# Kernel tuning notes

Measured on AMD Instinct MI355X. Metric: run time of the kernel, lower is better.

Reference implementation:

```python
import jax, jax.numpy as jnp
import numpy as np

B, S, D = 4, 1024, 768
V, L, K = 50265, 256, 4
COMMIT = 0.25
PERP_W = 0.1


def _l2n(a):
    return a * jax.lax.rsqrt(jnp.sum(a * a, axis=-1, keepdims=True) + 1e-12)


def setup_inputs() -> dict:
    key = jax.random.key(0)
    ks = jax.random.split(key, 4)
    return {
        'x': jax.random.normal(ks[0], (B, S, D), dtype=jnp.float32),
        'codebook': jax.random.normal(ks[1], (V, D), dtype=jnp.float32) * 0.02,
        'W_in': jax.random.normal(ks[2], (D, L), dtype=jnp.float32) / np.sqrt(D),
        'b_in': jnp.zeros((L,), dtype=jnp.float32),
        'W_code': jax.random.normal(ks[3], (D, L), dtype=jnp.float32) / np.sqrt(D),
        'b_code': jnp.zeros((L,), dtype=jnp.float32),
    }


def reference(x, codebook, W_in, b_in, W_code, b_code):
    # project inputs and codebook to latent space, L2-normalize
    zi = _l2n(x.reshape(-1, D) @ W_in + b_in)                 # [N, L]
    # original normalizes latent codebook twice (idempotent) then stop-grads
    zc = jax.lax.stop_gradient(_l2n(codebook @ W_code + b_code))  # [V, L]
    # squared euclidean distance: |a|^2 + |b|^2 - 2 a.b
    d = (jnp.sum(zi * zi, -1, keepdims=True)
         + jnp.sum(zc * zc, -1)[None, :]
         - 2.0 * (zi @ zc.T)).reshape(B, S, V)                # [B, S, V]
    # top-k nearest codes (exact top_k as reference for approx_min_k)
    idx = jax.lax.top_k(-d, K)[1]                             # [B, S, K] int32
    # quantize: gather codes and average over k (top_k_avg path)
    quantized = jnp.take(codebook, idx, axis=0).mean(axis=-2) # [B, S, D]
    # codebook stats without materializing [B,S,K,V] one-hot
    counts = jnp.zeros((V,), x.dtype).at[idx.reshape(-1)].add(1.0)
    codebook_usage = jnp.sum(counts > 0).astype(x.dtype) / V / K
    avg_probs = counts / (B * S * K)
    log_perp = -jnp.sum(avg_probs * jnp.log(avg_probs + 1e-10))
    perplexity = jnp.exp(log_perp)
    # train losses (quantized is stop-gradient'd before loss in original)
    q_sg = jax.lax.stop_gradient(quantized)

    def train_loss(q, t):
        e = jnp.mean((jax.lax.stop_gradient(q) - t) ** 2) * COMMIT
        ql = jnp.mean((q - jax.lax.stop_gradient(t)) ** 2)
        return e + ql

    loss = train_loss(q_sg, x)
    loss = loss + train_loss(q_sg @ W_code + b_code, x @ W_in + b_in)
    loss = loss + PERP_W * log_perp
    # straight-through estimator
    out = x + jax.lax.stop_gradient(q_sg - x)
    return out, loss, perplexity, codebook_usage
```

## Files before the change

kernel.cpp:

```cpp
#include <hip/hip_runtime.h>
#include <math.h>

#define N_TOK 4096
#define DDIM  768
#define LDIM  256
#define VNUM  50265
#define VPAD  50304
#define NT64  786
#define NGRP  16
#define QBLK  256
#define KSEL  4
#define M3    3145728

#define WS_ZI_PRE 0
#define WS_ZI     (WS_ZI_PRE + N_TOK*LDIM)
#define WS_ZC     (WS_ZI + N_TOK*LDIM)
#define WS_ZCB    (WS_ZC + VPAD*LDIM)
#define WS_QUANT  WS_ZCB
#define WS_CAND   (WS_ZCB + VPAD*LDIM/2)
#define WS_IDX    (WS_CAND + N_TOK*64)
#define WS_COUNTS (WS_IDX + N_TOK*4)
#define WS_ACCUM  (WS_COUNTS + VPAD)

typedef __attribute__((ext_vector_type(8))) short short8;
typedef __attribute__((ext_vector_type(4))) float f32x4;

__device__ __forceinline__ unsigned short f2bf(float f) {
    unsigned u = __float_as_uint(f);
    u += 0x7fffu + ((u >> 16) & 1u);
    return (unsigned short)(u >> 16);
}

__device__ __forceinline__ bool better(float v1, int i1, float v2, int i2) {
    return (v1 > v2) || (v1 == v2 && i1 < i2);
}

template<int K>
__device__ __forceinline__ void insertK(float (&v)[K], int (&ix)[K], float nv, int ni) {
    if (!better(nv, ni, v[K-1], ix[K-1])) return;
    v[K-1] = nv; ix[K-1] = ni;
    #pragma unroll
    for (int j = K-1; j > 0; j--) {
        if (better(v[j], ix[j], v[j-1], ix[j-1])) {
            float tv = v[j]; v[j] = v[j-1]; v[j-1] = tv;
            int ti = ix[j]; ix[j] = ix[j-1]; ix[j-1] = ti;
        } else break;
    }
}

__global__ __launch_bounds__(256) void gemm_k(
    const float* __restrict__ A, const float* __restrict__ W,
    const float* __restrict__ bias, float* __restrict__ out_pre,
    float* __restrict__ out_norm, unsigned short* __restrict__ out_bf,
    const float* __restrict__ target, float* __restrict__ accum_slot,
    int M, int mode)
{
    __shared__ float a_s[32*64];
    __shared__ float w_s[32*256];
    const int tid = threadIdx.x;
    const int tx = tid & 31, ty = tid >> 5;
    const int mbase = blockIdx.x * 64;

    float acc[8][8];
    #pragma unroll
    for (int i = 0; i < 8; i++)
        #pragma unroll
        for (int j = 0; j < 8; j++) acc[i][j] = 0.f;

    for (int kk = 0; kk < DDIM; kk += 32) {
        __syncthreads();
        #pragma unroll
        for (int s = 0; s < 2; s++) {
            int slot = tid + s*256;
            int row = slot >> 3, kc = (slot & 7) << 2;
            int gr = mbase + row; if (gr >= M) gr = M - 1;
            float4 v = *(const float4*)&A[(size_t)gr*DDIM + kk + kc];
            a_s[(kc+0)*64 + row] = v.x;
            a_s[(kc+1)*64 + row] = v.y;
            a_s[(kc+2)*64 + row] = v.z;
            a_s[(kc+3)*64 + row] = v.w;
        }
        #pragma unroll
        for (int s = 0; s < 8; s++) {
            int slot = tid + s*256;
            int r = slot >> 6, c = (slot & 63) << 2;
            *(float4*)&w_s[r*256 + c] = *(const float4*)&W[(size_t)(kk + r)*LDIM + c];
        }
        __syncthreads();
        #pragma unroll
        for (int k = 0; k < 32; k++) {
            float4 a0 = *(float4*)&a_s[k*64 + ty*8];
            float4 a1 = *(float4*)&a_s[k*64 + ty*8 + 4];
            float4 w0 = *(float4*)&w_s[k*256 + tx*4];
            float4 w1 = *(float4*)&w_s[k*256 + 128 + tx*4];
            float am[8] = {a0.x,a0.y,a0.z,a0.w,a1.x,a1.y,a1.z,a1.w};
            float wn[8] = {w0.x,w0.y,w0.z,w0.w,w1.x,w1.y,w1.z,w1.w};
            #pragma unroll
            for (int i = 0; i < 8; i++)
                #pragma unroll
                for (int j = 0; j < 8; j++)
                    acc[i][j] = fmaf(am[i], wn[j], acc[i][j]);
        }
    }

    float bn[8];
    #pragma unroll
    for (int j = 0; j < 8; j++) {
        int col = (j < 4) ? (tx*4 + j) : (128 + tx*4 + (j-4));
        bn[j] = bias[col];
    }
    #pragma unroll
    for (int i = 0; i < 8; i++)
        #pragma unroll
        for (int j = 0; j < 8; j++) acc[i][j] += bn[j];

    if (mode == 1) {
        #pragma unroll
        for (int i = 0; i < 8; i++) {
            int gr = mbase + ty*8 + i;
            if (gr < M) {
                *(float4*)&out_pre[(size_t)gr*LDIM + tx*4] =
                    make_float4(acc[i][0], acc[i][1], acc[i][2], acc[i][3]);
                *(float4*)&out_pre[(size_t)gr*LDIM + 128 + tx*4] =
                    make_float4(acc[i][4], acc[i][5], acc[i][6], acc[i][7]);
            }
        }
    }
    if (mode == 1 || mode == 2) {
        #pragma unroll
        for (int i = 0; i < 8; i++) {
            float s = 0.f;
            #pragma unroll
            for (int j = 0; j < 8; j++) s += acc[i][j]*acc[i][j];
            #pragma unroll
            for (int m = 16; m >= 1; m >>= 1) s += __shfl_xor(s, m, 64);
            float sc = 1.0f / sqrtf(s + 1e-12f);
            int gr = mbase + ty*8 + i;
            bool wr = (mode == 2) || (gr < M);
            if (wr) {
                float p[8];
                #pragma unroll
                for (int j = 0; j < 8; j++) p[j] = acc[i][j]*sc;
                *(float4*)&out_norm[(size_t)gr*LDIM + tx*4] = make_float4(p[0],p[1],p[2],p[3]);
                *(float4*)&out_norm[(size_t)gr*LDIM + 128 + tx*4] = make_float4(p[4],p[5],p[6],p[7]);
                if (out_bf) {
                    ushort4 b0, b1;
                    b0.x = f2bf(p[0]); b0.y = f2bf(p[1]); b0.z = f2bf(p[2]); b0.w = f2bf(p[3]);
                    b1.x = f2bf(p[4]); b1.y = f2bf(p[5]); b1.z = f2bf(p[6]); b1.w = f2bf(p[7]);
                    *(ushort4*)&out_bf[(size_t)gr*LDIM + tx*4] = b0;
                    *(ushort4*)&out_bf[(size_t)gr*LDIM + 128 + tx*4] = b1;
                }
            }
        }
    }
    if (mode == 3) {
        float ls = 0.f;
        #pragma unroll
        for (int i = 0; i < 8; i++) {
            int gr = mbase + ty*8 + i;
            if (gr < M) {
                #pragma unroll
                for (int j = 0; j < 8; j++) {
                    int col = (j < 4) ? (tx*4 + j) : (128 + tx*4 + (j-4));
                    float dd = acc[i][j] - target[(size_t)gr*LDIM + col];
                    ls = fmaf(dd, dd, ls);
                }
            }
        }
        #pragma unroll
        for (int off = 32; off >= 1; off >>= 1) ls += __shfl_down(ls, off, 64);
        __syncthreads();
        if ((tid & 63) == 0) a_s[tid >> 6] = ls;
        __syncthreads();
        if (tid == 0) atomicAdd(accum_slot, a_s[0]+a_s[1]+a_s[2]+a_s[3]);
    }
}


__device__ __forceinline__ void stage_chunk(
    const unsigned short* __restrict__ zcb, unsigned char* smem,
    int ci, int wave, int lane, int g)
{
    const int T  = g + (ci >> 2) * NGRP;
    const int kc = ci & 3;
    const int r_local = wave*8 + (lane >> 3);
    const int sg = (lane & 7) ^ (lane >> 3);
    const unsigned short* gp = zcb + (size_t)(T*64 + r_local)*LDIM + kc*64 + sg*8;
    unsigned char* lp = smem + (ci & 3)*8192 + wave*1024 + lane*16;
    __builtin_amdgcn_global_load_lds(
        (const __attribute__((address_space(1))) void*)gp,
        (__attribute__((address_space(3))) void*)lp, 16, 0, 0);
}

__global__ __launch_bounds__(512, 2) void filter_kernel(
    const float* __restrict__ zi, const unsigned short* __restrict__ zcb,
    int* __restrict__ cand)
{
    __shared__ unsigned char smem[32768];
    const int tid = threadIdx.x;
    const int wave = tid >> 6, lane = tid & 63;
    const int l15 = lane & 15, l4 = lane >> 4;
    const int qbase = blockIdx.x * QBLK + wave * 32;
    const int g = blockIdx.y;

    short8 afrag[2][8];
    #pragma unroll
    for (int qt = 0; qt < 2; qt++)
        #pragma unroll
        for (int ks = 0; ks < 8; ks++) {
            const float* src = zi + (size_t)(qbase + qt*16 + l15)*LDIM + ks*32 + l4*8;
            float4 v0 = *(const float4*)src;
            float4 v1 = *(const float4*)(src + 4);
            short8 a;
            a[0] = (short)f2bf(v0.x); a[1] = (short)f2bf(v0.y);
            a[2] = (short)f2bf(v0.z); a[3] = (short)f2bf(v0.w);
            a[4] = (short)f2bf(v1.x); a[5] = (short)f2bf(v1.y);
            a[6] = (short)f2bf(v1.z); a[7] = (short)f2bf(v1.w);
            afrag[qt][ks] = a;
        }

    float tv[2][4][3]; int tix[2][4][3];
    #pragma unroll
    for (int qt = 0; qt < 2; qt++)
        #pragma unroll
        for (int rr = 0; rr < 4; rr++)
            #pragma unroll
            for (int j = 0; j < 3; j++) { tv[qt][rr][j] = -1e30f; tix[qt][rr][j] = 0x7fffffff; }

    f32x4 acc[2][4];
    #pragma unroll
    for (int qt = 0; qt < 2; qt++)
        #pragma unroll
        for (int tc = 0; tc < 4; tc++) acc[qt][tc] = (f32x4)(0.f);

    const int nct = (g < 2) ? 50 : 49;
    const int NCk = nct * 4;

    stage_chunk(zcb, smem, 0, wave, lane, g);
    stage_chunk(zcb, smem, 1, wave, lane, g);
    stage_chunk(zcb, smem, 2, wave, lane, g);

    for (int ci = 0; ci < NCk; ci++) {
        __builtin_amdgcn_s_waitcnt(0x0F72);
        __builtin_amdgcn_s_barrier();
        asm volatile("" ::: "memory");
        int nx = ci + 3; if (nx >= NCk) nx -= NCk;
        stage_chunk(zcb, smem, nx, wave, lane, g);

        const unsigned short* lb = (const unsigned short*)(smem + (ci & 3)*8192);
        const int kc = ci & 3;
        #pragma unroll
        for (int ks2 = 0; ks2 < 2; ks2++) {
            const int kf = kc*2 + ks2;
            #pragma unroll
            for (int tc = 0; tc < 4; tc++) {
                const int c = tc*16 + l15;
                const int slot = (ks2*4 + l4) ^ (c & 7);
                const short8 b = *(const short8*)&lb[c*64 + slot*8];
                acc[0][tc] = __builtin_amdgcn_mfma_f32_16x16x32_bf16(afrag[0][kf], b, acc[0][tc], 0, 0, 0);
                acc[1][tc] = __builtin_amdgcn_mfma_f32_16x16x32_bf16(afrag[1][kf], b, acc[1][tc], 0, 0, 0);
            }
        }

        if ((ci & 3) == 3) {
            const int T = g + (ci >> 2)*NGRP;
            #pragma unroll
            for (int tc = 0; tc < 4; tc++) {
                const int col = T*64 + tc*16 + l15;
                const bool ok = col < VNUM;
                #pragma unroll
                for (int qt = 0; qt < 2; qt++) {
                    #pragma unroll
                    for (int rr = 0; rr < 4; rr++) {
                        float v = acc[qt][tc][rr];
                        if (ok) insertK<3>(tv[qt][rr], tix[qt][rr], v, col);
                    }
                    acc[qt][tc] = (f32x4)(0.f);
                }
            }
        }
    }

    #pragma unroll
    for (int qt = 0; qt < 2; qt++)
        #pragma unroll
        for (int rr = 0; rr < 4; rr++) {
            float mv[4] = { tv[qt][rr][0], tv[qt][rr][1], tv[qt][rr][2], -1e30f };
            int   mi[4] = { tix[qt][rr][0], tix[qt][rr][1], tix[qt][rr][2], 0x7fffffff };
            #pragma unroll
            for (int m = 1; m < 16; m <<= 1) {
                float ov[4]; int oi[4];
                #pragma unroll
                for (int s = 0; s < 4; s++) {
                    ov[s] = __shfl_xor(mv[s], m, 64);
                    oi[s] = __shfl_xor(mi[s], m, 64);
                }
                #pragma unroll
                for (int s = 0; s < 4; s++) insertK<4>(mv, mi, ov[s], oi[s]);
            }
            if (l15 == 0) {
                const int q = qbase + qt*16 + l4*4 + rr;
                #pragma unroll
                for (int j = 0; j < 4; j++) cand[(size_t)q*64 + g*4 + j] = mi[j];
            }
        }
}

__global__ __launch_bounds__(256) void rescore_kernel(
    const float* __restrict__ zi, const float* __restrict__ zc,
    const int* __restrict__ cand, int* __restrict__ idx4)
{
    __shared__ float zi_s[256];
    __shared__ float sval[64];
    __shared__ int   sidx[64];
    const int q = blockIdx.x;
    const int t = threadIdx.x;
    if (t < 64) *(float4*)&zi_s[t*4] = *(const float4*)&zi[(size_t)q*LDIM + t*4];
    __syncthreads();

    const int j = t >> 2, l4 = t & 3;
    int idx = cand[(size_t)q*64 + j];
    const bool valid = (unsigned)idx < (unsigned)VNUM;
    const float* r = zc + (size_t)(valid ? idx : 0)*LDIM;
    float dot = 0.f, nsq = 0.f;
    #pragma unroll
    for (int i = 0; i < 16; i++) {
        float4 v = *(const float4*)&r[i*16 + l4*4];
        float4 z = *(const float4*)&zi_s[i*16 + l4*4];
        dot = fmaf(v.x, z.x, fmaf(v.y, z.y, fmaf(v.z, z.z, fmaf(v.w, z.w, dot))));
        nsq = fmaf(v.x, v.x, fmaf(v.y, v.y, fmaf(v.z, v.z, fmaf(v.w, v.w, nsq))));
    }
    dot += __shfl_xor(dot, 1, 64); dot += __shfl_xor(dot, 2, 64);
    nsq += __shfl_xor(nsq, 1, 64); nsq += __shfl_xor(nsq, 2, 64);
    const float sc = valid ? (dot - 0.5f*nsq) : -1e30f;
    if (l4 == 0) { sval[j] = sc; sidx[j] = valid ? idx : 0x7fffffff; }
    __syncthreads();

    if (t < 64) {
        float v[4] = {-1e30f, -1e30f, -1e30f, -1e30f};
        int ix[4] = {0x7fffffff, 0x7fffffff, 0x7fffffff, 0x7fffffff};
        insertK<4>(v, ix, sval[t], sidx[t]);
        #pragma unroll
        for (int m = 1; m < 64; m <<= 1) {
            float ov[4]; int oi[4];
            #pragma unroll
            for (int s = 0; s < 4; s++) {
                ov[s] = __shfl_xor(v[s], m, 64);
                oi[s] = __shfl_xor(ix[s], m, 64);
            }
            #pragma unroll
            for (int s = 0; s < 4; s++) insertK<4>(v, ix, ov[s], oi[s]);
        }
        if (t == 0) {
            #pragma unroll
            for (int s = 0; s < 4; s++) idx4[q*4 + s] = ix[s];
        }
    }
}

__global__ __launch_bounds__(192) void gather_kernel(
    const float* __restrict__ x, const float* __restrict__ cb,
    const int* __restrict__ idx4, float* __restrict__ quant,
    float* __restrict__ out, float* __restrict__ counts,
    float* __restrict__ accum)
{
    __shared__ float red[3];
    const int n = blockIdx.x;
    const int t = threadIdx.x;
    const int i0 = idx4[n*4+0], i1 = idx4[n*4+1], i2 = idx4[n*4+2], i3 = idx4[n*4+3];
    if (t < 4) atomicAdd(&counts[idx4[n*4+t]], 1.0f);
    const int d = t*4;
    float4 c0 = *(const float4*)&cb[(size_t)i0*DDIM + d];
    float4 c1 = *(const float4*)&cb[(size_t)i1*DDIM + d];
    float4 c2 = *(const float4*)&cb[(size_t)i2*DDIM + d];
    float4 c3 = *(const float4*)&cb[(size_t)i3*DDIM + d];
    float4 xv = *(const float4*)&x[(size_t)n*DDIM + d];
    float4 qv;
    qv.x = (((c0.x + c1.x) + c2.x) + c3.x) * 0.25f;
    qv.y = (((c0.y + c1.y) + c2.y) + c3.y) * 0.25f;
    qv.z = (((c0.z + c1.z) + c2.z) + c3.z) * 0.25f;
    qv.w = (((c0.w + c1.w) + c2.w) + c3.w) * 0.25f;
    float4 o;
    o.x = xv.x + (qv.x - xv.x);
    o.y = xv.y + (qv.y - xv.y);
    o.z = xv.z + (qv.z - xv.z);
    o.w = xv.w + (qv.w - xv.w);
    *(float4*)&quant[(size_t)n*DDIM + d] = qv;
    *(float4*)&out[(size_t)n*DDIM + d] = o;
    float d0 = qv.x - xv.x, d1 = qv.y - xv.y, d2 = qv.z - xv.z, d3 = qv.w - xv.w;
    float ls = d0*d0 + d1*d1 + d2*d2 + d3*d3;
    #pragma unroll
    for (int off = 32; off >= 1; off >>= 1) ls += __shfl_down(ls, off, 64);
    if ((t & 63) == 0) red[t >> 6] = ls;
    __syncthreads();
    if (t == 0) atomicAdd(accum, red[0] + red[1] + red[2]);
}

__global__ __launch_bounds__(256) void stats_kernel(
    const float* __restrict__ counts, float* __restrict__ accum)
{
    __shared__ float redE[4], redN[4];
    int v = blockIdx.x*256 + threadIdx.x;
    float ent = 0.f, nnz = 0.f;
    if (v < VNUM) {
        float c = counts[v];
        if (c > 0.f) {
            float p = c * (1.0f/16384.0f);
            ent = p * logf(p + 1e-10f);
            nnz = 1.f;
        }
    }
    #pragma unroll
    for (int off = 32; off >= 1; off >>= 1) {
        ent += __shfl_down(ent, off, 64);
        nnz += __shfl_down(nnz, off, 64);
    }
    int t = threadIdx.x;
    if ((t & 63) == 0) { redE[t>>6] = ent; redN[t>>6] = nnz; }
    __syncthreads();
    if (t == 0) {
        atomicAdd(accum+2, redE[0]+redE[1]+redE[2]+redE[3]);
        atomicAdd(accum+3, redN[0]+redN[1]+redN[2]+redN[3]);
    }
}

__global__ void final_kernel(const float* __restrict__ accum, float* __restrict__ out)
{
    float logp = -accum[2];
    float m1 = accum[0] * (1.0f / (float)M3);
    float m2 = accum[1] * (1.0f / (float)(N_TOK*LDIM));
    float loss = (m1*0.25f + m1) + (m2*0.25f + m2) + 0.1f*logp;
    out[M3+0] = loss;
    out[M3+1] = expf(logp);
    out[M3+2] = (accum[3] / (float)VNUM) / (float)KSEL;
}

extern "C" void kernel_launch(void* const* d_in, const int* in_sizes, int n_in,
                              void* d_out, int out_size, void* d_ws, size_t ws_size,
                              hipStream_t stream)
{
    const float* x      = (const float*)d_in[0];
    const float* cb     = (const float*)d_in[1];
    const float* W_in   = (const float*)d_in[2];
    const float* b_in   = (const float*)d_in[3];
    const float* W_code = (const float*)d_in[4];
    const float* b_code = (const float*)d_in[5];
    float* out = (float*)d_out;
    float* w   = (float*)d_ws;

    float* zi_pre = w + WS_ZI_PRE;
    float* zi     = w + WS_ZI;
    float* zc     = w + WS_ZC;
    unsigned short* zcb = (unsigned short*)(w + WS_ZCB);
    float* quant  = w + WS_QUANT;
    int*   cand   = (int*)(w + WS_CAND);
    int*   idx4   = (int*)(w + WS_IDX);
    float* counts = w + WS_COUNTS;
    float* accum  = w + WS_ACCUM;

    hipMemsetAsync(counts, 0, (VPAD + 8)*sizeof(float), stream);

    gemm_k<<<N_TOK/64, 256, 0, stream>>>(x, W_in, b_in, zi_pre, zi, nullptr,
                                         nullptr, nullptr, N_TOK, 1);
    gemm_k<<<VPAD/64, 256, 0, stream>>>(cb, W_code, b_code, nullptr, zc, zcb,
                                        nullptr, nullptr, VNUM, 2);
    filter_kernel<<<dim3(N_TOK/QBLK, NGRP), 512, 0, stream>>>(zi, zcb, cand);
    rescore_kernel<<<N_TOK, 256, 0, stream>>>(zi, zc, cand, idx4);
    gather_kernel<<<N_TOK, 192, 0, stream>>>(x, cb, idx4, quant, out, counts, accum);
    stats_kernel<<<(VNUM + 255)/256, 256, 0, stream>>>(counts, accum);
    gemm_k<<<N_TOK/64, 256, 0, stream>>>(quant, W_code, b_code, nullptr, nullptr, nullptr,
                                         zi_pre, accum+1, N_TOK, 3);
    final_kernel<<<1, 1, 0, stream>>>(accum, out);
}
```

Measured before the change: 1.269 ms.

## Pre-swizzle codebook bf16 tiles and use register-staged double-buffered LDS in filter

The codebook projection GEMM now writes bf16 latents already in the per-chunk swizzled 64x64 tile layout, so each filter chunk becomes one contiguous 8KB block. The filter kernel drops the 4-deep async global_load_lds pipeline in favour of a 2-buffer LDS ring fed through registers, with two barriers per chunk. The input projection also emits a bf16 copy of the normalized latents, so the filter loads A fragments directly instead of converting from fp32. This trades the async direct-to-LDS path for simpler, fully coalesced loads, at the cost of more barriers and a shallower prefetch.

Result: faster. 1.240 ms (-2.2%).

```diff
diff --git a/kernel.cpp b/kernel.cpp
--- a/kernel.cpp
+++ b/kernel.cpp
@@ -14,7 +14,8 @@
 
 #define WS_ZI_PRE 0
 #define WS_ZI     (WS_ZI_PRE + N_TOK*LDIM)
-#define WS_ZC     (WS_ZI + N_TOK*LDIM)
+#define WS_ZIB    (WS_ZI + N_TOK*LDIM)
+#define WS_ZC     (WS_ZIB + N_TOK*LDIM/2)
 #define WS_ZCB    (WS_ZC + VPAD*LDIM)
 #define WS_QUANT  WS_ZCB
 #define WS_CAND   (WS_ZCB + VPAD*LDIM/2)
@@ -147,8 +148,20 @@
                     ushort4 b0, b1;
                     b0.x = f2bf(p[0]); b0.y = f2bf(p[1]); b0.z = f2bf(p[2]); b0.w = f2bf(p[3]);
                     b1.x = f2bf(p[4]); b1.y = f2bf(p[5]); b1.z = f2bf(p[6]); b1.w = f2bf(p[7]);
-                    *(ushort4*)&out_bf[(size_t)gr*LDIM + tx*4] = b0;
-                    *(ushort4*)&out_bf[(size_t)gr*LDIM + 128 + tx*4] = b1;
+                    if (mode == 1) {
+                        *(ushort4*)&out_bf[(size_t)gr*LDIM + tx*4] = b0;
+                        *(ushort4*)&out_bf[(size_t)gr*LDIM + 128 + tx*4] = b1;
+                    } else {
+                        const int T = gr >> 6, c = gr & 63;
+                        #pragma unroll
+                        for (int h = 0; h < 2; h++) {
+                            const int k0 = h*128 + tx*4;
+                            const int kc = k0 >> 6, seg = (k0 >> 3) & 7, e = k0 & 7;
+                            const int slot = c*8 + (seg ^ (c & 7));
+                            size_t idx = ((size_t)(T*4 + kc))*4096 + slot*8 + e;
+                            *(ushort4*)&out_bf[idx] = h ? b1 : b0;
+                        }
+                    }
                 }
             }
         }
@@ -176,27 +189,12 @@
     }
 }
 
-
-__device__ __forceinline__ void stage_chunk(
-    const unsigned short* __restrict__ zcb, unsigned char* smem,
-    int ci, int wave, int lane, int g)
-{
-    const int T  = g + (ci >> 2) * NGRP;
-    const int kc = ci & 3;
-    const int r_local = wave*8 + (lane >> 3);
-    const int sg = (lane & 7) ^ (lane >> 3);
-    const unsigned short* gp = zcb + (size_t)(T*64 + r_local)*LDIM + kc*64 + sg*8;
-    unsigned char* lp = smem + (ci & 3)*8192 + wave*1024 + lane*16;
-    __builtin_amdgcn_global_load_lds(
-        (const __attribute__((address_space(1))) void*)gp,
-        (__attribute__((address_space(3))) void*)lp, 16, 0, 0);
-}
-
-__global__ __launch_bounds__(512, 2) void filter_kernel(
-    const float* __restrict__ zi, const unsigned short* __restrict__ zcb,
+__global__ __launch_bounds__(512, 2) __attribute__((amdgpu_waves_per_eu(2, 2)))
+void filter_kernel(
+    const unsigned short* __restrict__ zib, const unsigned short* __restrict__ zcb,
     int* __restrict__ cand)
 {
-    __shared__ unsigned char smem[32768];
+    __shared__ unsigned short lds[2*4096];
     const int tid = threadIdx.x;
     const int wave = tid >> 6, lane = tid & 63;
     const int l15 = lane & 15, l4 = lane >> 4;
@@ -207,17 +205,8 @@
     #pragma unroll
     for (int qt = 0; qt < 2; qt++)
         #pragma unroll
-        for (int ks = 0; ks < 8; ks++) {
-            const float* src = zi + (size_t)(qbase + qt*16 + l15)*LDIM + ks*32 + l4*8;
-            float4 v0 = *(const float4*)src;
-            float4 v1 = *(const float4*)(src + 4);
-            short8 a;
-            a[0] = (short)f2bf(v0.x); a[1] = (short)f2bf(v0.y);
-            a[2] = (short)f2bf(v0.z); a[3] = (short)f2bf(v0.w);
-            a[4] = (short)f2bf(v1.x); a[5] = (short)f2bf(v1.y);
-            a[6] = (short)f2bf(v1.z); a[7] = (short)f2bf(v1.w);
-            afrag[qt][ks] = a;
-        }
+        for (int ks = 0; ks < 8; ks++)
+            afrag[qt][ks] = *(const short8*)&zib[(size_t)(qbase + qt*16 + l15)*LDIM + ks*32 + l4*8];
 
     float tv[2][4][3]; int tix[2][4][3];
     #pragma unroll
@@ -236,27 +225,23 @@
     const int nct = (g < 2) ? 50 : 49;
     const int NCk = nct * 4;
 
-    stage_chunk(zcb, smem, 0, wave, lane, g);
-    stage_chunk(zcb, smem, 1, wave, lane, g);
-    stage_chunk(zcb, smem, 2, wave, lane, g);
+    #define CHUNK_OFF(ci) ((size_t)((g + ((ci) >> 2)*NGRP)*4 + ((ci) & 3)) * 4096)
+
+    uint4 breg = *(const uint4*)&zcb[CHUNK_OFF(0) + tid*8];
+    *(uint4*)&lds[tid*8] = breg;
+    breg = *(const uint4*)&zcb[CHUNK_OFF(1) + tid*8];
+    __syncthreads();
 
     for (int ci = 0; ci < NCk; ci++) {
-        __builtin_amdgcn_s_waitcnt(0x0F72);
-        __builtin_amdgcn_s_barrier();
-        asm volatile("" ::: "memory");
-        int nx = ci + 3; if (nx >= NCk) nx -= NCk;
-        stage_chunk(zcb, smem, nx, wave, lane, g);
-
-        const unsigned short* lb = (const unsigned short*)(smem + (ci & 3)*8192);
-        const int kc = ci & 3;
+        const unsigned short* lb = &lds[(ci & 1)*4096];
         #pragma unroll
         for (int ks2 = 0; ks2 < 2; ks2++) {
-            const int kf = kc*2 + ks2;
+            const int kf = (ci & 3)*2 + ks2;
             #pragma unroll
             for (int tc = 0; tc < 4; tc++) {
                 const int c = tc*16 + l15;
-                const int slot = (ks2*4 + l4) ^ (c & 7);
-                const short8 b = *(const short8*)&lb[c*64 + slot*8];
+                const int slot = c*8 + ((ks2*4 + l4) ^ (c & 7));
+                const short8 b = *(const short8*)&lb[slot*8];
                 acc[0][tc] = __builtin_amdgcn_mfma_f32_16x16x32_bf16(afrag[0][kf], b, acc[0][tc], 0, 0, 0);
                 acc[1][tc] = __builtin_amdgcn_mfma_f32_16x16x32_bf16(afrag[1][kf], b, acc[1][tc], 0, 0, 0);
             }
@@ -279,7 +264,15 @@
                 }
             }
         }
-    }
+
+        __syncthreads();
+        if (ci + 1 < NCk) {
+            *(uint4*)&lds[((ci+1) & 1)*4096 + tid*8] = breg;
+            if (ci + 2 < NCk) breg = *(const uint4*)&zcb[CHUNK_OFF(ci+2) + tid*8];
+            __syncthreads();
+        }
+    }
+    #undef CHUNK_OFF
 
     #pragma unroll
     for (int qt = 0; qt < 2; qt++)
@@ -450,6 +443,7 @@
 
     float* zi_pre = w + WS_ZI_PRE;
     float* zi     = w + WS_ZI;
+    unsigned short* zib = (unsigned short*)(w + WS_ZIB);
     float* zc     = w + WS_ZC;
     unsigned short* zcb = (unsigned short*)(w + WS_ZCB);
     float* quant  = w + WS_QUANT;
@@ -460,11 +454,11 @@
 
     hipMemsetAsync(counts, 0, (VPAD + 8)*sizeof(float), stream);
 
-    gemm_k<<<N_TOK/64, 256, 0, stream>>>(x, W_in, b_in, zi_pre, zi, nullptr,
+    gemm_k<<<N_TOK/64, 256, 0, stream>>>(x, W_in, b_in, zi_pre, zi, zib,
                                          nullptr, nullptr, N_TOK, 1);
     gemm_k<<<VPAD/64, 256, 0, stream>>>(cb, W_code, b_code, nullptr, zc, zcb,
                                         nullptr, nullptr, VNUM, 2);
-    filter_kernel<<<dim3(N_TOK/QBLK, NGRP), 512, 0, stream>>>(zi, zcb, cand);
+    filter_kernel<<<dim3(N_TOK/QBLK, NGRP), 512, 0, stream>>>(zib, zcb, cand);
     rescore_kernel<<<N_TOK, 256, 0, stream>>>(zi, zc, cand, idx4);
     gather_kernel<<<N_TOK, 192, 0, stream>>>(x, cb, idx4, quant, out, counts, accum);
     stats_kernel<<<(VNUM + 255)/256, 256, 0, stream>>>(counts, accum);
```
